# Kernel optimization log

Hardware: AMD Instinct MI355X
Metric: run time of the kernel (lower is better)

## Reference

```python
import jax, jax.numpy as jnp
import numpy as np

B, N, M, D = 32, 500, 500, 256
SQRT_D = 16.0
LOGIT_CLIP = 10.0


def setup_inputs() -> dict:
    key = jax.random.key(0)
    ks = jax.random.split(key, 12)
    s = 1.0 / np.sqrt(D)
    return {
        "encoded_q0": jax.random.normal(ks[0], (B, N, D), jnp.float32),
        "encoded_jobs": jax.random.normal(ks[1], (B, M, D), jnp.float32),
        "encoded_q1": jax.random.normal(ks[2], (B, N, D), jnp.float32),
        "cur_cost_mat": jax.random.uniform(ks[3], (B, N, M), jnp.float32),
        "log_scale": jnp.ones((1,), jnp.float32),
        "ninf_mask": jnp.zeros((B, N, M), jnp.float32),
        "Wq0": jax.random.normal(ks[4], (D, D), jnp.float32) * s,
        "Wq1": jax.random.normal(ks[5], (D, D), jnp.float32) * s,
        "Wk": jax.random.normal(ks[6], (D, D), jnp.float32) * s,
        "Wv": jax.random.normal(ks[7], (D, D), jnp.float32) * s,
        "alpha1": jnp.ones((1,), jnp.float32),
        "alpha2": jnp.ones((1,), jnp.float32),
    }


def reference(encoded_q0, encoded_jobs, encoded_q1, cur_cost_mat, log_scale,
              ninf_mask, Wq0, Wq1, Wk, Wv, alpha1, alpha2):
    # precomputed state (set_kv / set_q1): Linear without bias -> x @ W.T
    k = jnp.einsum('bmd,ed->bme', encoded_jobs, Wk)
    v = jnp.einsum('bmd,ed->bme', encoded_jobs, Wv)
    q1 = jnp.einsum('bnd,ed->bne', encoded_q1, Wq1)
    q0 = jnp.einsum('bnd,ed->bne', encoded_q0, Wq0)
    q = q1 + q0

    # AAFM: adaptation bias = -alpha1 * log_scale * cost (+ ninf_mask)
    exp_bias = jnp.exp(-alpha1 * log_scale * cur_cost_mat + ninf_mask)  # (B,N,M)
    exp_k = jnp.exp(k)                                                   # (B,M,D)
    num = jnp.einsum('bnm,bmd->bnd', exp_bias, exp_k * v)
    den = jnp.einsum('bnm,bmd->bnd', exp_bias, exp_k)
    weighted = jnp.nan_to_num(num / den)
    aafm_out = jax.nn.sigmoid(q) * weighted                              # (B,N,D)

    # single-head scoring against raw encoded_jobs
    score = jnp.einsum('bnd,bmd->bnm', aafm_out, encoded_jobs)
    score = score / SQRT_D - alpha2 * log_scale * cur_cost_mat
    score = LOGIT_CLIP * jnp.tanh(score) + ninf_mask
    return jax.nn.softmax(score, axis=-1)
```

## Files before the change

kernel.cpp:

```cpp
#include <hip/hip_runtime.h>
#include <math.h>

using u16 = unsigned short;
typedef __attribute__((ext_vector_type(8))) short short8;
typedef __attribute__((ext_vector_type(16))) float floatx16;

constexpr int Bc = 32, Nn = 500, Mm = 500, Dd = 256;
constexpr float LOGIT_CLIP = 10.0f;
constexpr float INV_SQRT_D = 1.0f / 16.0f;

__device__ __forceinline__ floatx16 mfma32(short8 a, short8 b, floatx16 c) {
    return __builtin_amdgcn_mfma_f32_32x32x16_bf16(a, b, c, 0, 0, 0);
}

__device__ __forceinline__ floatx16 zero16() {
    floatx16 v = {0.f,0.f,0.f,0.f,0.f,0.f,0.f,0.f,0.f,0.f,0.f,0.f,0.f,0.f,0.f,0.f};
    return v;
}

__device__ __forceinline__ void split1(float x, u16& h, u16& l) {
    unsigned u = __float_as_uint(x);
    unsigned rh = (u + 0x7FFFu + ((u >> 16) & 1u)) & 0xFFFF0000u;
    float fh = __uint_as_float(rh);
    float fl = x - fh;
    unsigned ul = __float_as_uint(fl);
    unsigned rl = ul + 0x7FFFu + ((ul >> 16) & 1u);
    h = (u16)(rh >> 16);
    l = (u16)(rl >> 16);
}

__device__ __forceinline__ u16 bf16rtn(float x) {
    unsigned u = __float_as_uint(x);
    return (u16)((u + 0x7FFFu + ((u >> 16) & 1u)) >> 16);
}

__device__ __forceinline__ float fast_tanh(float x) {
    return 1.0f - 2.0f / (__expf(2.0f * x) + 1.0f);
}

__device__ __forceinline__ void split8(const float4& a, const float4& c,
                                       short8& hv, short8& lv) {
    u16 hh, ll;
    split1(a.x, hh, ll); hv[0] = (short)hh; lv[0] = (short)ll;
    split1(a.y, hh, ll); hv[1] = (short)hh; lv[1] = (short)ll;
    split1(a.z, hh, ll); hv[2] = (short)hh; lv[2] = (short)ll;
    split1(a.w, hh, ll); hv[3] = (short)hh; lv[3] = (short)ll;
    split1(c.x, hh, ll); hv[4] = (short)hh; lv[4] = (short)ll;
    split1(c.y, hh, ll); hv[5] = (short)hh; lv[5] = (short)ll;
    split1(c.z, hh, ll); hv[6] = (short)hh; lv[6] = (short)ll;
    split1(c.w, hh, ll); hv[7] = (short)hh; lv[7] = (short)ll;
}


__global__ __launch_bounds__(256) void k0w_pk(const float* __restrict__ s0,
                                              const float* __restrict__ s1,
                                              const float* __restrict__ s2,
                                              const float* __restrict__ s3,
                                              u16* __restrict__ pkw) {
    const float* s = blockIdx.y == 0 ? s0 : blockIdx.y == 1 ? s1 :
                     blockIdx.y == 2 ? s2 : s3;
    const int w = blockIdx.y;
    const int flat = (blockIdx.x * 256 + threadIdx.x) * 8;
    const int i = flat >> 8, j0 = flat & 255;
    float4 a = *(const float4*)&s[flat];
    float4 c = *(const float4*)&s[flat + 4];
    short8 hv, lv;
    split8(a, c, hv, lv);
    const int dt = i >> 5, i31 = i & 31, dc = j0 >> 4, hp = (j0 >> 3) & 1;
    const size_t off = (size_t)(w * 8 + dt) * 16384 + (size_t)dc * 1024
                     + (size_t)((hp << 5) | i31) * 8;
    *(short8*)&pkw[off] = hv;
    *(short8*)&pkw[off + 512] = lv;
}

__global__ __launch_bounds__(256) void k0pkj(const float* __restrict__ s,
                                             u16* __restrict__ d) {
    const int bx = blockIdx.x;
    const int b = bx >> 6;
    const int chunk = bx & 63;
    const int flat = threadIdx.x * 8;
    const int lr = flat >> 8;
    const int j0 = flat & 255;
    const int pr = chunk * 8 + lr;
    short8 hv = {0,0,0,0,0,0,0,0}, lv = {0,0,0,0,0,0,0,0};
    if (pr < Nn) {
        const size_t o = ((size_t)b * Nn + pr) * Dd + j0;
        float4 a = *(const float4*)&s[o];
        float4 c = *(const float4*)&s[o + 4];
        split8(a, c, hv, lv);
    }
    const int mt = pr >> 5, r31 = pr & 31;
    const int dc = j0 >> 4, hp = (j0 >> 3) & 1;
    const size_t off = (size_t)(b * 16 + mt) * 16384 + (size_t)dc * 1024
                     + (size_t)((hp << 5) | r31) * 8;
    *(short8*)&d[off] = hv;
    *(short8*)&d[off + 512] = lv;
}

__global__ __launch_bounds__(256) void k1_kv(const u16* __restrict__ pkj,
                                             const u16* __restrict__ pkw,
                                             u16* __restrict__ pkb) {
    const int lane = threadIdx.x & 63, wv = threadIdx.x >> 6;
    const int l31 = lane & 31, h = lane >> 5;
    const int b = blockIdx.z;
    const int dt = blockIdx.y * 4 + wv;
    const int mt = blockIdx.x;
    const int M0 = mt * 32;

    const size_t wk  = (size_t)dt * 16384 + (size_t)lane * 8;
    const size_t wvb = (size_t)(8 + dt) * 16384 + (size_t)lane * 8;
    const size_t jb  = (size_t)(b * 16 + mt) * 16384 + (size_t)lane * 8;

    floatx16 ak = zero16(), av = zero16();

    short8 buf[3][6];
#define K1L(S, DC) { \
    buf[S][0] = *(const short8*)(pkw + wk  + (size_t)(DC) * 1024); \
    buf[S][1] = *(const short8*)(pkw + wk  + (size_t)(DC) * 1024 + 512); \
    buf[S][2] = *(const short8*)(pkw + wvb + (size_t)(DC) * 1024); \
    buf[S][3] = *(const short8*)(pkw + wvb + (size_t)(DC) * 1024 + 512); \
    buf[S][4] = *(const short8*)(pkj + jb  + (size_t)(DC) * 1024); \
    buf[S][5] = *(const short8*)(pkj + jb  + (size_t)(DC) * 1024 + 512); }

    K1L(0, 0)
    K1L(1, 1)
#pragma unroll
    for (int it = 0; it < 16; ++it) {
        if (it + 2 < 16) { K1L((it + 2) % 3, it + 2) }
        const int c = it % 3;
        ak = mfma32(buf[c][0], buf[c][4], ak);
        ak = mfma32(buf[c][0], buf[c][5], ak);
        ak = mfma32(buf[c][1], buf[c][4], ak);
        av = mfma32(buf[c][2], buf[c][4], av);
        av = mfma32(buf[c][2], buf[c][5], av);
        av = mfma32(buf[c][3], buf[c][4], av);
    }
#undef K1L

    const int hp = (l31 >> 3) & 1, ee = l31 & 7, mcl = l31 >> 4;
    const size_t sb0 = ((size_t)b * 8 + dt) * 65536
                     + (size_t)(mt * 2 + mcl) * 2048 + (size_t)hp * 256 + ee;
    const bool v0 = (M0 + l31) < Mm;
#pragma unroll
    for (int r = 0; r < 16; ++r) {
        const int d31 = (r & 3) + ((r >> 2) << 3) + (h << 2);
        const size_t o = sb0 + (size_t)d31 * 8;
        u16 hh, ll;
        const float ek = v0 ? __expf(ak[r]) : 0.f;
        const float ev = v0 ? ek * av[r] : 0.f;
        split1(ek, hh, ll); pkb[o] = hh; pkb[o + 512] = ll;
        split1(ev, hh, ll); pkb[o + 1024] = hh; pkb[o + 1536] = ll;
    }
}

__global__ __launch_bounds__(256) void k2_q(const float* __restrict__ q0,
                                            const float* __restrict__ q1,
                                            const u16* __restrict__ pkw,
                                            float* __restrict__ sq) {
    __shared__ u16 tq[4][32][264];
    const int t = threadIdx.x;
    const int lane = t & 63, wv = t >> 6;
    const int l31 = lane & 31, h = lane >> 5;
    const int b = blockIdx.y;
    const int nt = blockIdx.x;

#pragma unroll
    for (int s = 0; s < 2; ++s) {
        const float* src = s ? q1 : q0;
#pragma unroll
        for (int it = 0; it < 4; ++it) {
            const int flat = (it * 256 + t) * 8;
            const int nl = flat >> 8, j0 = flat & 255;
            const int n = min(nt * 32 + nl, Nn - 1);
            const size_t o = ((size_t)b * Nn + n) * Dd + j0;
            float4 a = *(const float4*)&src[o];
            float4 c = *(const float4*)&src[o + 4];
            short8 hv, lv;
            split8(a, c, hv, lv);
            *(short8*)&tq[s * 2][nl][j0] = hv;
            *(short8*)&tq[s * 2 + 1][nl][j0] = lv;
        }
    }
    __syncthreads();

    const int dt0 = wv;
    const int dt1 = wv + 4;
    const size_t w00 = (size_t)(16 + dt0) * 16384 + (size_t)lane * 8;
    const size_t w10 = (size_t)(24 + dt0) * 16384 + (size_t)lane * 8;
    const size_t w01 = (size_t)(16 + dt1) * 16384 + (size_t)lane * 8;
    const size_t w11 = (size_t)(24 + dt1) * 16384 + (size_t)lane * 8;

    floatx16 acc0 = zero16(), acc1 = zero16();

    short8 buf[3][8];
#define K2L(S, DC) { \
    buf[S][0] = *(const short8*)(pkw + w00 + (size_t)(DC) * 1024); \
    buf[S][1] = *(const short8*)(pkw + w00 + (size_t)(DC) * 1024 + 512); \
    buf[S][2] = *(const short8*)(pkw + w10 + (size_t)(DC) * 1024); \
    buf[S][3] = *(const short8*)(pkw + w10 + (size_t)(DC) * 1024 + 512); \
    buf[S][4] = *(const short8*)(pkw + w01 + (size_t)(DC) * 1024); \
    buf[S][5] = *(const short8*)(pkw + w01 + (size_t)(DC) * 1024 + 512); \
    buf[S][6] = *(const short8*)(pkw + w11 + (size_t)(DC) * 1024); \
    buf[S][7] = *(const short8*)(pkw + w11 + (size_t)(DC) * 1024 + 512); }

    K2L(0, 0)
    K2L(1, 1)
#pragma unroll
    for (int it = 0; it < 16; ++it) {
        if (it + 2 < 16) { K2L((it + 2) % 3, it + 2) }
        const int c = it % 3;
        const int co = it * 16 + h * 8;
        short8 a0h = *(const short8*)&tq[0][l31][co];
        short8 a0l = *(const short8*)&tq[1][l31][co];
        short8 a1h = *(const short8*)&tq[2][l31][co];
        short8 a1l = *(const short8*)&tq[3][l31][co];
        acc0 = mfma32(a0h, buf[c][0], acc0);
        acc0 = mfma32(a0h, buf[c][1], acc0);
        acc0 = mfma32(a0l, buf[c][0], acc0);
        acc0 = mfma32(a1h, buf[c][2], acc0);
        acc0 = mfma32(a1h, buf[c][3], acc0);
        acc0 = mfma32(a1l, buf[c][2], acc0);
        acc1 = mfma32(a0h, buf[c][4], acc1);
        acc1 = mfma32(a0h, buf[c][5], acc1);
        acc1 = mfma32(a0l, buf[c][4], acc1);
        acc1 = mfma32(a1h, buf[c][6], acc1);
        acc1 = mfma32(a1h, buf[c][7], acc1);
        acc1 = mfma32(a1l, buf[c][6], acc1);
    }
#undef K2L

    float* sp0 = sq + ((((size_t)b * 16 + nt) * 8 + dt0) * 64 + lane) * 16;
    float* sp1 = sq + ((((size_t)b * 16 + nt) * 8 + dt1) * 64 + lane) * 16;
#pragma unroll
    for (int r = 0; r < 16; ++r) {
        sp0[r] = 1.0f / (1.0f + __expf(-acc0[r]));
        sp1[r] = 1.0f / (1.0f + __expf(-acc1[r]));
    }
}

__global__ __launch_bounds__(512) void k34(const float* __restrict__ cost,
                                           const float* __restrict__ mask,
                                           const float* __restrict__ alpha1,
                                           const float* __restrict__ alpha2,
                                           const float* __restrict__ lsc,
                                           const u16* __restrict__ pkb,
                                           const u16* __restrict__ pkj,
                                           const float* __restrict__ sq,
                                           float* __restrict__ out) {
    __shared__ u16 sh[16640];
    __shared__ float pred[32][8];
    const int i = blockIdx.x;
    const int x = i & 7, j = i >> 3;
    const int nt = j & 15;
    const int b = ((j >> 4) << 3) + x;
    const int t = threadIdx.x;
    const int lane = t & 63, wv = t >> 6;
    const int l31 = lane & 31, h = lane >> 5;
    const int N0 = nt << 5;

    const float a1ls = alpha1[0] * lsc[0];
#pragma unroll
    for (int q = 0; q < 4; ++q) {
        const int flat = (q << 12) + (t << 3);
        const int nl = flat >> 9, m = flat & 511;
        const int n = min(N0 + nl, Nn - 1);
        const size_t o = ((size_t)b * Nn + n) * Mm + m;
        ushort4 w0 = {0, 0, 0, 0}, w1 = {0, 0, 0, 0};
        if (m <= 488) {
            float4 c0 = *(const float4*)&cost[o];
            float4 c1 = *(const float4*)&cost[o + 4];
            float4 k0 = *(const float4*)&mask[o];
            float4 k1 = *(const float4*)&mask[o + 4];
            w0.x = bf16rtn(__expf(fmaf(-a1ls, c0.x, k0.x)));
            w0.y = bf16rtn(__expf(fmaf(-a1ls, c0.y, k0.y)));
            w0.z = bf16rtn(__expf(fmaf(-a1ls, c0.z, k0.z)));
            w0.w = bf16rtn(__expf(fmaf(-a1ls, c0.w, k0.w)));
            w1.x = bf16rtn(__expf(fmaf(-a1ls, c1.x, k1.x)));
            w1.y = bf16rtn(__expf(fmaf(-a1ls, c1.y, k1.y)));
            w1.z = bf16rtn(__expf(fmaf(-a1ls, c1.z, k1.z)));
            w1.w = bf16rtn(__expf(fmaf(-a1ls, c1.w, k1.w)));
        } else if (m == 496) {
            float4 c0 = *(const float4*)&cost[o];
            float4 k0 = *(const float4*)&mask[o];
            w0.x = bf16rtn(__expf(fmaf(-a1ls, c0.x, k0.x)));
            w0.y = bf16rtn(__expf(fmaf(-a1ls, c0.y, k0.y)));
            w0.z = bf16rtn(__expf(fmaf(-a1ls, c0.z, k0.z)));
            w0.w = bf16rtn(__expf(fmaf(-a1ls, c0.w, k0.w)));
        }
        *(ushort4*)&sh[nl * 520 + m] = w0;
        *(ushort4*)&sh[nl * 520 + m + 4] = w1;
    }
    __syncthreads();

    const size_t bbase = ((size_t)b * 8 + wv) * 65536 + (size_t)lane * 8;
    floatx16 dn = zero16(), nm = zero16();
    short8 buf[3][4];
#define K3L(S, MC) { \
    buf[S][0] = *(const short8*)(pkb + bbase + (size_t)(MC) * 2048); \
    buf[S][1] = *(const short8*)(pkb + bbase + (size_t)(MC) * 2048 + 512); \
    buf[S][2] = *(const short8*)(pkb + bbase + (size_t)(MC) * 2048 + 1024); \
    buf[S][3] = *(const short8*)(pkb + bbase + (size_t)(MC) * 2048 + 1536); }

    K3L(0, 0)
    K3L(1, 1)
#pragma unroll
    for (int mc = 0; mc < 32; ++mc) {
        if (mc + 2 < 32) { K3L((mc + 2) % 3, mc + 2) }
        const int c = mc % 3;
        short8 aa = *(const short8*)&sh[l31 * 520 + mc * 16 + h * 8];
        dn = mfma32(aa, buf[c][0], dn);
        dn = mfma32(aa, buf[c][1], dn);
        nm = mfma32(aa, buf[c][2], nm);
        nm = mfma32(aa, buf[c][3], nm);
    }
#undef K3L
    __syncthreads();

    {
        const float* sp = sq + ((((size_t)b * 16 + nt) * 8 + wv) * 64 + lane) * 16;
        const int hp = (l31 >> 3) & 1, ee = l31 & 7;
        const int fo = (wv * 2 + (l31 >> 4)) * 1024 + hp * 256 + ee;
#pragma unroll
        for (int r = 0; r < 16; ++r) {
            const int n31 = (r & 3) + ((r >> 2) << 3) + (h << 2);
            const float d0 = dn[r];
            const float w0 = (d0 != 0.f) ? nm[r] / d0 : 0.f;
            u16 hh, ll;
            split1(sp[r] * w0, hh, ll);
            sh[fo + n31 * 8] = hh;
            sh[fo + 512 + n31 * 8] = ll;
        }
    }
    __syncthreads();

    const u16* jb0p = pkj + ((size_t)b * 16 + wv * 2) * 16384 + (size_t)lane * 8;
    const u16* jb1p = jb0p + 16384;
    const int m0g = wv * 64 + l31;
    const int m1g = m0g + 32;

    floatx16 acc0 = zero16(), acc1 = zero16();
    short8 jbuf[3][4];
#define K4L(S, DC) { \
    jbuf[S][0] = *(const short8*)(jb0p + (size_t)(DC) * 1024); \
    jbuf[S][1] = *(const short8*)(jb0p + (size_t)(DC) * 1024 + 512); \
    jbuf[S][2] = *(const short8*)(jb1p + (size_t)(DC) * 1024); \
    jbuf[S][3] = *(const short8*)(jb1p + (size_t)(DC) * 1024 + 512); }

    K4L(0, 0)
    K4L(1, 1)
#pragma unroll
    for (int dc = 0; dc < 16; ++dc) {
        if (dc + 2 < 16) { K4L((dc + 2) % 3, dc + 2) }
        const int c = dc % 3;
        short8 aH = *(const short8*)&sh[dc * 1024 + lane * 8];
        short8 aL = *(const short8*)&sh[dc * 1024 + 512 + lane * 8];
        acc0 = mfma32(aH, jbuf[c][0], acc0);
        acc0 = mfma32(aH, jbuf[c][1], acc0);
        acc0 = mfma32(aL, jbuf[c][0], acc0);
        acc1 = mfma32(aH, jbuf[c][2], acc1);
        acc1 = mfma32(aH, jbuf[c][3], acc1);
        acc1 = mfma32(aL, jbuf[c][2], acc1);
    }
#undef K4L

    float lg0[16], lg1[16];
    const float a2ls = alpha2[0] * lsc[0];
    const size_t cb = (size_t)b * Nn * Mm;
#pragma unroll
    for (int r = 0; r < 16; ++r) {
        const int row = (r & 3) + ((r >> 2) << 3) + (h << 2);
        const int n = N0 + row;
        if (n < Nn) {
            const size_t o = cb + (size_t)n * Mm + m0g;
            lg0[r] = LOGIT_CLIP * fast_tanh(fmaf(-a2ls, cost[o], acc0[r] * INV_SQRT_D)) + mask[o];
            if (m1g < Mm) {
                const size_t o1 = o + 32;
                lg1[r] = LOGIT_CLIP * fast_tanh(fmaf(-a2ls, cost[o1], acc1[r] * INV_SQRT_D)) + mask[o1];
            } else lg1[r] = -1e30f;
        } else { lg0[r] = -1e30f; lg1[r] = -1e30f; }
    }

    float rm[16];
#pragma unroll
    for (int r = 0; r < 16; ++r) rm[r] = fmaxf(lg0[r], lg1[r]);
#pragma unroll
    for (int d = 1; d < 32; d <<= 1)
#pragma unroll
        for (int r = 0; r < 16; ++r) rm[r] = fmaxf(rm[r], __shfl_xor(rm[r], d));
    if (l31 == 0) {
#pragma unroll
        for (int r = 0; r < 16; ++r)
            pred[(r & 3) + ((r >> 2) << 3) + (h << 2)][wv] = rm[r];
    }
    __syncthreads();
    float fm[16];
#pragma unroll
    for (int r = 0; r < 16; ++r) {
        const int row = (r & 3) + ((r >> 2) << 3) + (h << 2);
        float v = pred[row][0];
#pragma unroll
        for (int w = 1; w < 8; ++w) v = fmaxf(v, pred[row][w]);
        fm[r] = v;
    }
    __syncthreads();

    float sm[16];
#pragma unroll
    for (int r = 0; r < 16; ++r) {
        lg0[r] = __expf(lg0[r] - fm[r]);
        lg1[r] = __expf(lg1[r] - fm[r]);
        sm[r] = lg0[r] + lg1[r];
    }
#pragma unroll
    for (int d = 1; d < 32; d <<= 1)
#pragma unroll
        for (int r = 0; r < 16; ++r) sm[r] += __shfl_xor(sm[r], d);
    if (l31 == 0) {
#pragma unroll
        for (int r = 0; r < 16; ++r)
            pred[(r & 3) + ((r >> 2) << 3) + (h << 2)][wv] = sm[r];
    }
    __syncthreads();

#pragma unroll
    for (int r = 0; r < 16; ++r) {
        const int row = (r & 3) + ((r >> 2) << 3) + (h << 2);
        const int n = N0 + row;
        if (n < Nn) {
            float s = pred[row][0];
#pragma unroll
            for (int w = 1; w < 8; ++w) s += pred[row][w];
            const float inv = 1.0f / s;
            const size_t o = cb + (size_t)n * Mm + m0g;
            out[o] = lg0[r] * inv;
            if (m1g < Mm) out[o + 32] = lg1[r] * inv;
        }
    }
}

extern "C" void kernel_launch(void* const* d_in, const int* in_sizes, int n_in,
                              void* d_out, int out_size, void* d_ws, size_t ws_size,
                              hipStream_t stream) {
    const float* q0        = (const float*)d_in[0];
    const float* jobs      = (const float*)d_in[1];
    const float* q1        = (const float*)d_in[2];
    const float* cost      = (const float*)d_in[3];
    const float* log_scale = (const float*)d_in[4];
    const float* mask      = (const float*)d_in[5];
    const float* Wq0       = (const float*)d_in[6];
    const float* Wq1       = (const float*)d_in[7];
    const float* Wk        = (const float*)d_in[8];
    const float* Wv        = (const float*)d_in[9];
    const float* alpha1    = (const float*)d_in[10];
    const float* alpha2    = (const float*)d_in[11];
    float* out = (float*)d_out;

    const size_t PK_SZ  = (size_t)Bc * 16 * 16384;
    const size_t PKW_SZ = (size_t)4 * 8 * 16384;
    const size_t PKB_SZ = (size_t)Bc * 8 * 65536;

    u16* ws   = (u16*)d_ws;
    u16* pkj  = ws;
    u16* pkw  = ws + PK_SZ;
    u16* pkb  = pkw + PKW_SZ;
    float* sq = (float*)(pkb + PKB_SZ);
    (void)ws_size;

    dim3 blk(256);
    k0w_pk<<<dim3(32, 4), blk, 0, stream>>>(Wk, Wv, Wq0, Wq1, pkw);
    k0pkj<<<2048, blk, 0, stream>>>(jobs, pkj);
    k1_kv<<<dim3(16, 2, 32), blk, 0, stream>>>(pkj, pkw, pkb);
    k2_q<<<dim3(16, 32), blk, 0, stream>>>(q0, q1, pkw, sq);
    k34<<<512, dim3(512), 0, stream>>>(cost, mask, alpha1, alpha2, log_scale,
                                       pkb, pkj, sq, out);
}
```

Before: 273.4 us.

## Fuse jobs packing into K/V projection kernel and widen Q kernel blocks

The separate jobs bf16-split packing kernel is removed. k1_kv now loads the jobs tile from global memory, splits it into shared memory, writes the packed copy for the later scoring kernel, and feeds the MFMAs from shared memory. This saves one launch and one global read of the packed jobs. Both k1_kv and k2_q move to 512-thread blocks with one 32-wide d-tile per wave instead of two per wave or per grid-y slice, so fewer blocks each do more work and per-wave register pressure drops. In exchange the packing work now runs on fewer blocks and k1_kv needs extra shared memory and a barrier.

```diff
diff --git a/kernel.cpp b/kernel.cpp
--- a/kernel.cpp
+++ b/kernel.cpp
@@ -73,54 +73,62 @@
     *(short8*)&pkw[off + 512] = lv;
 }
 
-__global__ __launch_bounds__(256) void k0pkj(const float* __restrict__ s,
-                                             u16* __restrict__ d) {
-    const int bx = blockIdx.x;
-    const int b = bx >> 6;
-    const int chunk = bx & 63;
-    const int flat = threadIdx.x * 8;
-    const int lr = flat >> 8;
-    const int j0 = flat & 255;
-    const int pr = chunk * 8 + lr;
-    short8 hv = {0,0,0,0,0,0,0,0}, lv = {0,0,0,0,0,0,0,0};
-    if (pr < Nn) {
-        const size_t o = ((size_t)b * Nn + pr) * Dd + j0;
-        float4 a = *(const float4*)&s[o];
-        float4 c = *(const float4*)&s[o + 4];
-        split8(a, c, hv, lv);
-    }
-    const int mt = pr >> 5, r31 = pr & 31;
-    const int dc = j0 >> 4, hp = (j0 >> 3) & 1;
-    const size_t off = (size_t)(b * 16 + mt) * 16384 + (size_t)dc * 1024
-                     + (size_t)((hp << 5) | r31) * 8;
-    *(short8*)&d[off] = hv;
-    *(short8*)&d[off + 512] = lv;
-}
-
-__global__ __launch_bounds__(256) void k1_kv(const u16* __restrict__ pkj,
+__global__ __launch_bounds__(512) void k1_kv(const float* __restrict__ jobs,
                                              const u16* __restrict__ pkw,
+                                             u16* __restrict__ pkj,
                                              u16* __restrict__ pkb) {
-    const int lane = threadIdx.x & 63, wv = threadIdx.x >> 6;
+    __shared__ u16 tq[2][32][264];
+    const int t = threadIdx.x;
+    const int lane = t & 63, wv = t >> 6;
     const int l31 = lane & 31, h = lane >> 5;
-    const int b = blockIdx.z;
-    const int dt = blockIdx.y * 4 + wv;
     const int mt = blockIdx.x;
+    const int b = blockIdx.y;
     const int M0 = mt * 32;
 
+#pragma unroll
+    for (int it = 0; it < 2; ++it) {
+        const int flat = (it * 512 + t) * 8;
+        const int nl = flat >> 8, j0 = flat & 255;
+        const int m = M0 + nl;
+        short8 hv = {0,0,0,0,0,0,0,0}, lv = {0,0,0,0,0,0,0,0};
+        if (m < Mm) {
+            const size_t o = ((size_t)b * Mm + m) * Dd + j0;
+            float4 a = *(const float4*)&jobs[o];
+            float4 c = *(const float4*)&jobs[o + 4];
+            split8(a, c, hv, lv);
+        }
+        *(short8*)&tq[0][nl][j0] = hv;
+        *(short8*)&tq[1][nl][j0] = lv;
+    }
+    __syncthreads();
+
+    {
+        u16* dst = pkj + (size_t)(b * 16 + mt) * 16384;
+#pragma unroll
+        for (int it = 0; it < 4; ++it) {
+            const int u = it * 512 + t;
+            const int dc = u >> 7;
+            const int rem = u & 127;
+            const int sel = rem >> 6;
+            const int idx = rem & 63;
+            const int hp = idx >> 5, r31 = idx & 31;
+            short8 v = *(const short8*)&tq[sel][r31][dc * 16 + hp * 8];
+            *(short8*)&dst[(size_t)dc * 1024 + sel * 512 + (size_t)idx * 8] = v;
+        }
+    }
+
+    const int dt = wv;
     const size_t wk  = (size_t)dt * 16384 + (size_t)lane * 8;
     const size_t wvb = (size_t)(8 + dt) * 16384 + (size_t)lane * 8;
-    const size_t jb  = (size_t)(b * 16 + mt) * 16384 + (size_t)lane * 8;
 
     floatx16 ak = zero16(), av = zero16();
 
-    short8 buf[3][6];
+    short8 buf[3][4];
 #define K1L(S, DC) { \
     buf[S][0] = *(const short8*)(pkw + wk  + (size_t)(DC) * 1024); \
     buf[S][1] = *(const short8*)(pkw + wk  + (size_t)(DC) * 1024 + 512); \
     buf[S][2] = *(const short8*)(pkw + wvb + (size_t)(DC) * 1024); \
-    buf[S][3] = *(const short8*)(pkw + wvb + (size_t)(DC) * 1024 + 512); \
-    buf[S][4] = *(const short8*)(pkj + jb  + (size_t)(DC) * 1024); \
-    buf[S][5] = *(const short8*)(pkj + jb  + (size_t)(DC) * 1024 + 512); }
+    buf[S][3] = *(const short8*)(pkw + wvb + (size_t)(DC) * 1024 + 512); }
 
     K1L(0, 0)
     K1L(1, 1)
@@ -128,12 +136,15 @@
     for (int it = 0; it < 16; ++it) {
         if (it + 2 < 16) { K1L((it + 2) % 3, it + 2) }
         const int c = it % 3;
-        ak = mfma32(buf[c][0], buf[c][4], ak);
-        ak = mfma32(buf[c][0], buf[c][5], ak);
-        ak = mfma32(buf[c][1], buf[c][4], ak);
-        av = mfma32(buf[c][2], buf[c][4], av);
-        av = mfma32(buf[c][2], buf[c][5], av);
-        av = mfma32(buf[c][3], buf[c][4], av);
+        const int co = it * 16 + h * 8;
+        short8 jH = *(const short8*)&tq[0][l31][co];
+        short8 jL = *(const short8*)&tq[1][l31][co];
+        ak = mfma32(buf[c][0], jH, ak);
+        ak = mfma32(buf[c][0], jL, ak);
+        ak = mfma32(buf[c][1], jH, ak);
+        av = mfma32(buf[c][2], jH, av);
+        av = mfma32(buf[c][2], jL, av);
+        av = mfma32(buf[c][3], jH, av);
     }
 #undef K1L
 
@@ -153,7 +164,7 @@
     }
 }
 
-__global__ __launch_bounds__(256) void k2_q(const float* __restrict__ q0,
+__global__ __launch_bounds__(512) void k2_q(const float* __restrict__ q0,
                                             const float* __restrict__ q1,
                                             const u16* __restrict__ pkw,
                                             float* __restrict__ sq) {
@@ -168,8 +179,8 @@
     for (int s = 0; s < 2; ++s) {
         const float* src = s ? q1 : q0;
 #pragma unroll
-        for (int it = 0; it < 4; ++it) {
-            const int flat = (it * 256 + t) * 8;
+        for (int it = 0; it < 2; ++it) {
+            const int flat = (it * 512 + t) * 8;
             const int nl = flat >> 8, j0 = flat & 255;
             const int n = min(nt * 32 + nl, Nn - 1);
             const size_t o = ((size_t)b * Nn + n) * Dd + j0;
@@ -183,25 +194,18 @@
     }
     __syncthreads();
 
-    const int dt0 = wv;
-    const int dt1 = wv + 4;
-    const size_t w00 = (size_t)(16 + dt0) * 16384 + (size_t)lane * 8;
-    const size_t w10 = (size_t)(24 + dt0) * 16384 + (size_t)lane * 8;
-    const size_t w01 = (size_t)(16 + dt1) * 16384 + (size_t)lane * 8;
-    const size_t w11 = (size_t)(24 + dt1) * 16384 + (size_t)lane * 8;
-
-    floatx16 acc0 = zero16(), acc1 = zero16();
-
-    short8 buf[3][8];
+    const int dt = wv;
+    const size_t w0b = (size_t)(16 + dt) * 16384 + (size_t)lane * 8;
+    const size_t w1b = (size_t)(24 + dt) * 16384 + (size_t)lane * 8;
+
+    floatx16 acc = zero16();
+
+    short8 buf[3][4];
 #define K2L(S, DC) { \
-    buf[S][0] = *(const short8*)(pkw + w00 + (size_t)(DC) * 1024); \
-    buf[S][1] = *(const short8*)(pkw + w00 + (size_t)(DC) * 1024 + 512); \
-    buf[S][2] = *(const short8*)(pkw + w10 + (size_t)(DC) * 1024); \
-    buf[S][3] = *(const short8*)(pkw + w10 + (size_t)(DC) * 1024 + 512); \
-    buf[S][4] = *(const short8*)(pkw + w01 + (size_t)(DC) * 1024); \
-    buf[S][5] = *(const short8*)(pkw + w01 + (size_t)(DC) * 1024 + 512); \
-    buf[S][6] = *(const short8*)(pkw + w11 + (size_t)(DC) * 1024); \
-    buf[S][7] = *(const short8*)(pkw + w11 + (size_t)(DC) * 1024 + 512); }
+    buf[S][0] = *(const short8*)(pkw + w0b + (size_t)(DC) * 1024); \
+    buf[S][1] = *(const short8*)(pkw + w0b + (size_t)(DC) * 1024 + 512); \
+    buf[S][2] = *(const short8*)(pkw + w1b + (size_t)(DC) * 1024); \
+    buf[S][3] = *(const short8*)(pkw + w1b + (size_t)(DC) * 1024 + 512); }
 
     K2L(0, 0)
     K2L(1, 1)
@@ -214,27 +218,19 @@
         short8 a0l = *(const short8*)&tq[1][l31][co];
         short8 a1h = *(const short8*)&tq[2][l31][co];
         short8 a1l = *(const short8*)&tq[3][l31][co];
-        acc0 = mfma32(a0h, buf[c][0], acc0);
-        acc0 = mfma32(a0h, buf[c][1], acc0);
-        acc0 = mfma32(a0l, buf[c][0], acc0);
-        acc0 = mfma32(a1h, buf[c][2], acc0);
-        acc0 = mfma32(a1h, buf[c][3], acc0);
-        acc0 = mfma32(a1l, buf[c][2], acc0);
-        acc1 = mfma32(a0h, buf[c][4], acc1);
-        acc1 = mfma32(a0h, buf[c][5], acc1);
-        acc1 = mfma32(a0l, buf[c][4], acc1);
-        acc1 = mfma32(a1h, buf[c][6], acc1);
-        acc1 = mfma32(a1h, buf[c][7], acc1);
-        acc1 = mfma32(a1l, buf[c][6], acc1);
+        acc = mfma32(a0h, buf[c][0], acc);
+        acc = mfma32(a0h, buf[c][1], acc);
+        acc = mfma32(a0l, buf[c][0], acc);
+        acc = mfma32(a1h, buf[c][2], acc);
+        acc = mfma32(a1h, buf[c][3], acc);
+        acc = mfma32(a1l, buf[c][2], acc);
     }
 #undef K2L
 
-    float* sp0 = sq + ((((size_t)b * 16 + nt) * 8 + dt0) * 64 + lane) * 16;
-    float* sp1 = sq + ((((size_t)b * 16 + nt) * 8 + dt1) * 64 + lane) * 16;
-#pragma unroll
-    for (int r = 0; r < 16; ++r) {
-        sp0[r] = 1.0f / (1.0f + __expf(-acc0[r]));
-        sp1[r] = 1.0f / (1.0f + __expf(-acc1[r]));
+    float* sp = sq + ((((size_t)b * 16 + nt) * 8 + dt) * 64 + lane) * 16;
+#pragma unroll
+    for (int r = 0; r < 16; ++r) {
+        sp[r] = 1.0f / (1.0f + __expf(-acc[r]));
     }
 }
 
@@ -466,11 +462,9 @@
     float* sq = (float*)(pkb + PKB_SZ);
     (void)ws_size;
 
-    dim3 blk(256);
-    k0w_pk<<<dim3(32, 4), blk, 0, stream>>>(Wk, Wv, Wq0, Wq1, pkw);
-    k0pkj<<<2048, blk, 0, stream>>>(jobs, pkj);
-    k1_kv<<<dim3(16, 2, 32), blk, 0, stream>>>(pkj, pkw, pkb);
-    k2_q<<<dim3(16, 32), blk, 0, stream>>>(q0, q1, pkw, sq);
+    k0w_pk<<<dim3(32, 4), dim3(256), 0, stream>>>(Wk, Wv, Wq0, Wq1, pkw);
+    k1_kv<<<dim3(16, 32), dim3(512), 0, stream>>>(jobs, pkw, pkj, pkb);
+    k2_q<<<dim3(16, 32), dim3(512), 0, stream>>>(q0, q1, pkw, sq);
     k34<<<512, dim3(512), 0, stream>>>(cost, mask, alpha1, alpha2, log_scale,
                                        pkb, pkj, sq, out);
 }
```

After: 263.9 us. 3.5% less time.
